# Kernel optimization log

Measured on AMD Instinct MI355X. Metric: run time of the kernel, lower is better.

## Reference

```python
import jax, jax.numpy as jnp
import numpy as np

B, N, D_MODEL, HIDDEN = 4, 1024, 1024, 1024
N_HEAD, D_KEY, D_VALUE = 16, 64, 64


def setup_inputs() -> dict:
    key = jax.random.key(0)
    ks = jax.random.split(key, 12)
    s = 0.02
    return {
        "queries": jax.random.normal(ks[0], (B, N, D_MODEL), jnp.float32),
        "keys": jax.random.normal(ks[1], (B, N, HIDDEN), jnp.float32),
        "values": jax.random.normal(ks[2], (B, N, HIDDEN), jnp.float32),
        "attn_bias": jax.random.normal(ks[3], (B, N_HEAD, N, N), jnp.float32),
        "Wq": jax.random.normal(ks[4], (D_MODEL, D_KEY * N_HEAD), jnp.float32) * s,
        "bq": jnp.zeros((D_KEY * N_HEAD,), jnp.float32),
        "Wk": jax.random.normal(ks[5], (HIDDEN, D_KEY * N_HEAD), jnp.float32) * s,
        "bk": jnp.zeros((D_KEY * N_HEAD,), jnp.float32),
        "Wv": jax.random.normal(ks[6], (HIDDEN, D_VALUE * N_HEAD), jnp.float32) * s,
        "bv": jnp.zeros((D_VALUE * N_HEAD,), jnp.float32),
        "Wo": jax.random.normal(ks[7], (max(D_MODEL, HIDDEN), D_MODEL), jnp.float32) * s,
        "bo": jnp.zeros((D_MODEL,), jnp.float32),
    }


def reference(queries, keys, values, attn_bias, Wq, bq, Wk, bk, Wv, bv, Wo, bo):
    b, n, _ = queries.shape
    # QKV projections, split heads -> [b, h, n, d]
    q = (queries @ Wq + bq).reshape(b, n, N_HEAD, D_KEY).transpose(0, 2, 1, 3)
    k = (keys @ Wk + bk).reshape(b, keys.shape[1], N_HEAD, D_KEY).transpose(0, 2, 1, 3)
    v = (values @ Wv + bv).reshape(b, values.shape[1], N_HEAD, D_VALUE).transpose(0, 2, 1, 3)
    # scaled dot-product attention with additive bias (dropout_rate=0 -> identity)
    scaled_q = q * (D_KEY ** -0.5)
    product = jnp.einsum("bhqd,bhkd->bhqk", scaled_q, k) + attn_bias
    weights = jax.nn.softmax(product, axis=-1)
    ctx = jnp.einsum("bhqk,bhkd->bhqd", weights, v)
    # combine heads -> [b, n, h*d]
    out = ctx.transpose(0, 2, 1, 3).reshape(b, n, N_HEAD * D_VALUE)
    return out @ Wo + bo
```

## Files before the change

### kernel.cpp

```cpp
#include <hip/hip_runtime.h>
#include <hip/hip_bf16.h>
#include <cstdint>
#include <type_traits>


typedef unsigned short u16;
typedef __attribute__((ext_vector_type(8))) short v8bf;
typedef __attribute__((ext_vector_type(4))) float v4f;

#define DEV static __device__ __forceinline__

DEV float b2f(u16 u) { union { uint32_t u; float f; } v; v.u = ((uint32_t)u) << 16; return v.f; }
DEV u16 f2b(float f) {
    union { float f; uint32_t u; } v; v.f = f;
    uint32_t r = v.u + 0x7FFFu + ((v.u >> 16) & 1u);
    return (u16)(r >> 16);
}

__global__ __launch_bounds__(256) void transpose_w(const float* __restrict__ in,
                                                   u16* __restrict__ out) {
    __shared__ float tile[32][33];
    const int tx = threadIdx.x, ty = threadIdx.y;
    const int n0 = blockIdx.x * 32, k0 = blockIdx.y * 32;
#pragma unroll
    for (int i = 0; i < 4; i++)
        tile[ty + i * 8][tx] = in[(size_t)(k0 + ty + i * 8) * 1024 + n0 + tx];
    __syncthreads();
#pragma unroll
    for (int i = 0; i < 4; i++)
        out[(size_t)(n0 + ty + i * 8) * 1024 + k0 + tx] = f2b(tile[tx][ty + i * 8]);
}

__global__ __launch_bounds__(256) void transpose_v(const u16* __restrict__ V,
                                                   u16* __restrict__ VT) {
    __shared__ u16 tile[32][33];
    const int tx = threadIdx.x, ty = threadIdx.y;
    const int n0 = blockIdx.x * 32, d0 = blockIdx.y * 32, bh = blockIdx.z;
    const int b = bh >> 4, h = bh & 15;
#pragma unroll
    for (int i = 0; i < 4; i++)
        tile[ty + i * 8][tx] = V[(size_t)(b * 1024 + n0 + ty + i * 8) * 1024 + h * 64 + d0 + tx];
    __syncthreads();
#pragma unroll
    for (int i = 0; i < 4; i++)
        VT[(size_t)(bh * 64 + d0 + ty + i * 8) * 1024 + n0 + tx] = tile[tx][ty + i * 8];
}

template <typename TA, typename TO>
__global__ __launch_bounds__(256) void gemm_nt(const TA* __restrict__ A,
                                               const u16* __restrict__ Bt,
                                               const float* __restrict__ bias,
                                               TO* __restrict__ C) {
    __shared__ __align__(16) u16 aS[128][72];
    __shared__ __align__(16) u16 bS[128][72];
    const int tid = threadIdx.x;
    const int wave = tid >> 6, lane = tid & 63;
    const int l16 = lane & 15, quad = lane >> 4;
    const int m0 = blockIdx.x * 128, n0 = blockIdx.y * 128;
    const int mb = (wave >> 1) * 64, nb = (wave & 1) * 64;

    v4f acc[4][4];
#pragma unroll
    for (int i = 0; i < 4; i++)
#pragma unroll
        for (int j = 0; j < 4; j++) acc[i][j] = (v4f){0.f, 0.f, 0.f, 0.f};

    for (int kk = 0; kk < 1024; kk += 64) {
        __syncthreads();
        if constexpr (std::is_same_v<TA, float>) {
#pragma unroll
            for (int i = 0; i < 8; i++) {
                const int idx = tid + 256 * i;
                const int row = idx >> 4, c4 = idx & 15;
                const float4 f = *reinterpret_cast<const float4*>(
                    &A[(size_t)(m0 + row) * 1024 + kk + c4 * 4]);
                union { u16 h[4]; uint2 v; } pk;
                pk.h[0] = f2b(f.x); pk.h[1] = f2b(f.y);
                pk.h[2] = f2b(f.z); pk.h[3] = f2b(f.w);
                *reinterpret_cast<uint2*>(&aS[row][c4 * 4]) = pk.v;
            }
        } else {
#pragma unroll
            for (int i = 0; i < 4; i++) {
                const int idx = tid + 256 * i;
                const int row = idx >> 3, off = idx & 7;
                *reinterpret_cast<int4*>(&aS[row][off * 8]) =
                    *reinterpret_cast<const int4*>(&A[(size_t)(m0 + row) * 1024 + kk + off * 8]);
            }
        }
#pragma unroll
        for (int i = 0; i < 4; i++) {
            const int idx = tid + 256 * i;
            const int row = idx >> 3, off = idx & 7;
            *reinterpret_cast<int4*>(&bS[row][off * 8]) =
                *reinterpret_cast<const int4*>(&Bt[(size_t)(n0 + row) * 1024 + kk + off * 8]);
        }
        __syncthreads();
#pragma unroll
        for (int kt = 0; kt < 2; kt++) {
            v8bf af[4], bfr[4];
#pragma unroll
            for (int i = 0; i < 4; i++) {
                af[i]  = *reinterpret_cast<const v8bf*>(&aS[mb + i * 16 + l16][kt * 32 + quad * 8]);
                bfr[i] = *reinterpret_cast<const v8bf*>(&bS[nb + i * 16 + l16][kt * 32 + quad * 8]);
            }
#pragma unroll
            for (int i = 0; i < 4; i++)
#pragma unroll
                for (int j = 0; j < 4; j++)
                    acc[i][j] = __builtin_amdgcn_mfma_f32_16x16x32_bf16(af[i], bfr[j], acc[i][j], 0, 0, 0);
        }
    }
    float bv[4];
#pragma unroll
    for (int j = 0; j < 4; j++) bv[j] = bias[n0 + nb + j * 16 + l16];
#pragma unroll
    for (int i = 0; i < 4; i++)
#pragma unroll
        for (int j = 0; j < 4; j++) {
            const int col = n0 + nb + j * 16 + l16;
#pragma unroll
            for (int r = 0; r < 4; r++) {
                const int row = m0 + mb + i * 16 + quad * 4 + r;
                const float val = acc[i][j][r] + bv[j];
                if constexpr (std::is_same_v<TO, u16>) C[(size_t)row * 1024 + col] = f2b(val);
                else                                   C[(size_t)row * 1024 + col] = val;
            }
        }
}

__global__ __launch_bounds__(256) void attn_kernel(const u16* __restrict__ Q,
                                                   const u16* __restrict__ K,
                                                   const u16* __restrict__ VT,
                                                   const float* __restrict__ bias,
                                                   u16* __restrict__ ctx) {
    __shared__ __align__(16) u16 kS[128][72];
    __shared__ __align__(16) u16 vS[64][136];
    __shared__ __align__(16) u16 pS[4][16][40];
    __shared__ float rsLDS[4][16];
    __shared__ float ctxLDS[4][16][64];

    const int tid = threadIdx.x;
    const int wave = tid >> 6, lane = tid & 63, l16 = lane & 15, quad = lane >> 4;
    const int q0 = blockIdx.x * 16;
    const int bh = blockIdx.y;
    const int b = bh >> 4, h = bh & 15;

    v8bf qf[2];
    {
        const size_t qrow = (size_t)(b * 1024 + q0 + l16) * 1024 + h * 64;
        qf[0] = *reinterpret_cast<const v8bf*>(&Q[qrow + quad * 8]);
        qf[1] = *reinterpret_cast<const v8bf*>(&Q[qrow + 32 + quad * 8]);
    }

    v4f ctxacc[4];
#pragma unroll
    for (int v = 0; v < 4; v++) ctxacc[v] = (v4f){0.f, 0.f, 0.f, 0.f};
    float rs[4] = {0.f, 0.f, 0.f, 0.f};

    const size_t kbase = (size_t)b * 1024 * 1024 + (size_t)h * 64;
    const size_t vtbase = (size_t)bh * 64 * 1024;
    const size_t bbase = ((size_t)bh * 1024 + q0) * 1024;

    for (int c = 0; c < 8; c++) {
        const int nc = c * 128;
        __syncthreads();
#pragma unroll
        for (int i = 0; i < 4; i++) {
            const int idx = tid + 256 * i;
            const int key = idx >> 3, off = idx & 7;
            *reinterpret_cast<int4*>(&kS[key][off * 8]) =
                *reinterpret_cast<const int4*>(&K[kbase + (size_t)(nc + key) * 1024 + off * 8]);
        }
#pragma unroll
        for (int i = 0; i < 4; i++) {
            const int idx = tid + 256 * i;
            const int d = idx >> 4, off = idx & 15;
            *reinterpret_cast<int4*>(&vS[d][off * 8]) =
                *reinterpret_cast<const int4*>(&VT[vtbase + (size_t)d * 1024 + nc + off * 8]);
        }
        __syncthreads();
#pragma unroll
        for (int t = 0; t < 2; t++) {
            v4f s = (v4f){0.f, 0.f, 0.f, 0.f};
#pragma unroll
            for (int kt = 0; kt < 2; kt++) {
                v8bf bfr = *reinterpret_cast<const v8bf*>(&kS[wave * 32 + t * 16 + l16][kt * 32 + quad * 8]);
                s = __builtin_amdgcn_mfma_f32_16x16x32_bf16(qf[kt], bfr, s, 0, 0, 0);
            }
            const int keyg = nc + wave * 32 + t * 16 + l16;
#pragma unroll
            for (int r = 0; r < 4; r++) {
                const float lg = s[r] * 0.125f + bias[bbase + (size_t)(quad * 4 + r) * 1024 + keyg];
                const float p = __expf(lg);
                rs[r] += p;
                pS[wave][quad * 4 + r][t * 16 + l16] = f2b(p);
            }
        }
        __syncthreads();
        {
            v8bf pf = *reinterpret_cast<const v8bf*>(&pS[wave][l16][quad * 8]);
#pragma unroll
            for (int v = 0; v < 4; v++) {
                v8bf vf = *reinterpret_cast<const v8bf*>(&vS[v * 16 + l16][wave * 32 + quad * 8]);
                ctxacc[v] = __builtin_amdgcn_mfma_f32_16x16x32_bf16(pf, vf, ctxacc[v], 0, 0, 0);
            }
        }
    }

#pragma unroll
    for (int r = 0; r < 4; r++) {
        float v = rs[r];
        v += __shfl_xor(v, 1, 16);
        v += __shfl_xor(v, 2, 16);
        v += __shfl_xor(v, 4, 16);
        v += __shfl_xor(v, 8, 16);
        rs[r] = v;
    }
    if (l16 == 0) {
#pragma unroll
        for (int r = 0; r < 4; r++) rsLDS[wave][quad * 4 + r] = rs[r];
    }
#pragma unroll
    for (int v = 0; v < 4; v++)
#pragma unroll
        for (int r = 0; r < 4; r++)
            ctxLDS[wave][quad * 4 + r][v * 16 + l16] = ctxacc[v][r];
    __syncthreads();
#pragma unroll
    for (int i = 0; i < 4; i++) {
        const int row = (tid >> 6) + 4 * i;
        const int d = tid & 63;
        const float sum = ctxLDS[0][row][d] + ctxLDS[1][row][d] + ctxLDS[2][row][d] + ctxLDS[3][row][d];
        const float den = rsLDS[0][row] + rsLDS[1][row] + rsLDS[2][row] + rsLDS[3][row];
        ctx[(size_t)(b * 1024 + q0 + row) * 1024 + h * 64 + d] = f2b(sum / den);
    }
}

extern "C" void kernel_launch(void* const* d_in, const int* in_sizes, int n_in,
                              void* d_out, int out_size, void* d_ws, size_t ws_size,
                              hipStream_t stream) {
    const float* queries = (const float*)d_in[0];
    const float* keys    = (const float*)d_in[1];
    const float* values  = (const float*)d_in[2];
    const float* abias   = (const float*)d_in[3];
    const float* Wq = (const float*)d_in[4];
    const float* bq = (const float*)d_in[5];
    const float* Wk = (const float*)d_in[6];
    const float* bk = (const float*)d_in[7];
    const float* Wv = (const float*)d_in[8];
    const float* bv = (const float*)d_in[9];
    const float* Wo = (const float*)d_in[10];
    const float* bo = (const float*)d_in[11];
    float* out = (float*)d_out;

    char* ws = (char*)d_ws;
    u16* Qb   = (u16*)(ws);
    u16* Kb   = (u16*)(ws + (size_t)(8u << 20));
    u16* Vb   = (u16*)(ws + (size_t)(16u << 20));
    u16* VTb  = (u16*)(ws + (size_t)(24u << 20));
    u16* ctxb = (u16*)(ws + (size_t)(32u << 20));
    u16* WqT  = (u16*)(ws + (size_t)(40u << 20));
    u16* WkT  = (u16*)(ws + (size_t)(42u << 20));
    u16* WvT  = (u16*)(ws + (size_t)(44u << 20));
    u16* WoT  = (u16*)(ws + (size_t)(46u << 20));

    dim3 tb(32, 8);
    transpose_w<<<dim3(32, 32), tb, 0, stream>>>(Wq, WqT);
    transpose_w<<<dim3(32, 32), tb, 0, stream>>>(Wk, WkT);
    transpose_w<<<dim3(32, 32), tb, 0, stream>>>(Wv, WvT);
    transpose_w<<<dim3(32, 32), tb, 0, stream>>>(Wo, WoT);

    gemm_nt<float, u16><<<dim3(32, 8), 256, 0, stream>>>(queries, WqT, bq, Qb);
    gemm_nt<float, u16><<<dim3(32, 8), 256, 0, stream>>>(keys,    WkT, bk, Kb);
    gemm_nt<float, u16><<<dim3(32, 8), 256, 0, stream>>>(values,  WvT, bv, Vb);

    transpose_v<<<dim3(32, 2, 64), tb, 0, stream>>>(Vb, VTb);

    attn_kernel<<<dim3(64, 64), 256, 0, stream>>>(Qb, Kb, VTb, abias, ctxb);

    gemm_nt<u16, float><<<dim3(32, 8), 256, 0, stream>>>(ctxb, WoT, bo, out);
}
```

Before: 586.6 us.

## Give each attention wave its own query rows and batch weight transposes and QKV GEMMs

The attention kernel now gives each block 64 query rows, with each wave owning 16 rows and sweeping all 128 keys of a chunk. This reuses every K/V tile loaded into LDS across four times more queries and drops the cross-wave LDS reduction of context and row sums. The four weight transposes become one launch and the three QKV GEMMs become one launch, cutting launch count and letting the blocks fill the device together. In exchange the attention grid shrinks four-fold to 1024 blocks, and per-wave register and LDS use grows.

```diff
diff --git a/kernel.cpp b/kernel.cpp
--- a/kernel.cpp
+++ b/kernel.cpp
@@ -17,9 +17,18 @@
     return (u16)(r >> 16);
 }
 
-__global__ __launch_bounds__(256) void transpose_w(const float* __restrict__ in,
-                                                   u16* __restrict__ out) {
+__global__ __launch_bounds__(256) void transpose_w4(const float* __restrict__ w0,
+                                                    const float* __restrict__ w1,
+                                                    const float* __restrict__ w2,
+                                                    const float* __restrict__ w3,
+                                                    u16* __restrict__ o0,
+                                                    u16* __restrict__ o1,
+                                                    u16* __restrict__ o2,
+                                                    u16* __restrict__ o3) {
     __shared__ float tile[32][33];
+    const int z = blockIdx.z;
+    const float* in = (z == 0) ? w0 : (z == 1) ? w1 : (z == 2) ? w2 : w3;
+    u16* out = (z == 0) ? o0 : (z == 1) ? o1 : (z == 2) ? o2 : o3;
     const int tx = threadIdx.x, ty = threadIdx.y;
     const int n0 = blockIdx.x * 32, k0 = blockIdx.y * 32;
 #pragma unroll
@@ -47,16 +56,14 @@
 }
 
 template <typename TA, typename TO>
-__global__ __launch_bounds__(256) void gemm_nt(const TA* __restrict__ A,
-                                               const u16* __restrict__ Bt,
-                                               const float* __restrict__ bias,
-                                               TO* __restrict__ C) {
+DEV void gemm_body(const TA* __restrict__ A, const u16* __restrict__ Bt,
+                   const float* __restrict__ bias, TO* __restrict__ C,
+                   int m0, int n0) {
     __shared__ __align__(16) u16 aS[128][72];
     __shared__ __align__(16) u16 bS[128][72];
     const int tid = threadIdx.x;
     const int wave = tid >> 6, lane = tid & 63;
     const int l16 = lane & 15, quad = lane >> 4;
-    const int m0 = blockIdx.x * 128, n0 = blockIdx.y * 128;
     const int mb = (wave >> 1) * 64, nb = (wave & 1) * 64;
 
     v4f acc[4][4];
@@ -129,38 +136,64 @@
         }
 }
 
+__global__ __launch_bounds__(256) void gemm_qkv(const float* __restrict__ q,
+                                                const float* __restrict__ k,
+                                                const float* __restrict__ v,
+                                                const u16* __restrict__ WqT,
+                                                const u16* __restrict__ WkT,
+                                                const u16* __restrict__ WvT,
+                                                const float* __restrict__ bq,
+                                                const float* __restrict__ bk,
+                                                const float* __restrict__ bv,
+                                                u16* __restrict__ Qb,
+                                                u16* __restrict__ Kb,
+                                                u16* __restrict__ Vb) {
+    const int z = blockIdx.z;
+    const float* A = (z == 0) ? q : (z == 1) ? k : v;
+    const u16* Bt  = (z == 0) ? WqT : (z == 1) ? WkT : WvT;
+    const float* bi = (z == 0) ? bq : (z == 1) ? bk : bv;
+    u16* C = (z == 0) ? Qb : (z == 1) ? Kb : Vb;
+    gemm_body<float, u16>(A, Bt, bi, C, blockIdx.x * 128, blockIdx.y * 128);
+}
+
+__global__ __launch_bounds__(256) void gemm_out(const u16* __restrict__ A,
+                                                const u16* __restrict__ Bt,
+                                                const float* __restrict__ bias,
+                                                float* __restrict__ C) {
+    gemm_body<u16, float>(A, Bt, bias, C, blockIdx.x * 128, blockIdx.y * 128);
+}
+
 __global__ __launch_bounds__(256) void attn_kernel(const u16* __restrict__ Q,
                                                    const u16* __restrict__ K,
                                                    const u16* __restrict__ VT,
                                                    const float* __restrict__ bias,
                                                    u16* __restrict__ ctx) {
     __shared__ __align__(16) u16 kS[128][72];
-    __shared__ __align__(16) u16 vS[64][136];
-    __shared__ __align__(16) u16 pS[4][16][40];
-    __shared__ float rsLDS[4][16];
-    __shared__ float ctxLDS[4][16][64];
+    __shared__ __align__(16) u16 vS[64][132];
+    __shared__ __align__(16) u16 pS[4][16][132];
 
     const int tid = threadIdx.x;
     const int wave = tid >> 6, lane = tid & 63, l16 = lane & 15, quad = lane >> 4;
-    const int q0 = blockIdx.x * 16;
+    const int q0 = blockIdx.x * 64;
     const int bh = blockIdx.y;
     const int b = bh >> 4, h = bh & 15;
+    const int qw = q0 + wave * 16;
 
     v8bf qf[2];
     {
-        const size_t qrow = (size_t)(b * 1024 + q0 + l16) * 1024 + h * 64;
+        const size_t qrow = (size_t)(b * 1024 + qw + l16) * 1024 + h * 64;
         qf[0] = *reinterpret_cast<const v8bf*>(&Q[qrow + quad * 8]);
         qf[1] = *reinterpret_cast<const v8bf*>(&Q[qrow + 32 + quad * 8]);
     }
 
-    v4f ctxacc[4];
-#pragma unroll
-    for (int v = 0; v < 4; v++) ctxacc[v] = (v4f){0.f, 0.f, 0.f, 0.f};
+    v4f ctxa[4];
+#pragma unroll
+    for (int dt = 0; dt < 4; dt++) ctxa[dt] = (v4f){0.f, 0.f, 0.f, 0.f};
     float rs[4] = {0.f, 0.f, 0.f, 0.f};
 
     const size_t kbase = (size_t)b * 1024 * 1024 + (size_t)h * 64;
     const size_t vtbase = (size_t)bh * 64 * 1024;
-    const size_t bbase = ((size_t)bh * 1024 + q0) * 1024;
+    const size_t bbase = ((size_t)bh * 1024 + qw) * 1024;
 
     for (int c = 0; c < 8; c++) {
         const int nc = c * 128;
@@ -181,14 +214,14 @@
         }
         __syncthreads();
 #pragma unroll
-        for (int t = 0; t < 2; t++) {
+        for (int t = 0; t < 8; t++) {
             v4f s = (v4f){0.f, 0.f, 0.f, 0.f};
 #pragma unroll
             for (int kt = 0; kt < 2; kt++) {
-                v8bf bfr = *reinterpret_cast<const v8bf*>(&kS[wave * 32 + t * 16 + l16][kt * 32 + quad * 8]);
+                v8bf bfr = *reinterpret_cast<const v8bf*>(&kS[t * 16 + l16][kt * 32 + quad * 8]);
                 s = __builtin_amdgcn_mfma_f32_16x16x32_bf16(qf[kt], bfr, s, 0, 0, 0);
             }
-            const int keyg = nc + wave * 32 + t * 16 + l16;
+            const int keyg = nc + t * 16 + l16;
 #pragma unroll
             for (int r = 0; r < 4; r++) {
                 const float lg = s[r] * 0.125f + bias[bbase + (size_t)(quad * 4 + r) * 1024 + keyg];
@@ -198,12 +231,13 @@
             }
         }
         __syncthreads();
-        {
-            v8bf pf = *reinterpret_cast<const v8bf*>(&pS[wave][l16][quad * 8]);
-#pragma unroll
-            for (int v = 0; v < 4; v++) {
-                v8bf vf = *reinterpret_cast<const v8bf*>(&vS[v * 16 + l16][wave * 32 + quad * 8]);
-                ctxacc[v] = __builtin_amdgcn_mfma_f32_16x16x32_bf16(pf, vf, ctxacc[v], 0, 0, 0);
+#pragma unroll
+        for (int kt = 0; kt < 4; kt++) {
+            v8bf pf = *reinterpret_cast<const v8bf*>(&pS[wave][l16][kt * 32 + quad * 8]);
+#pragma unroll
+            for (int dt = 0; dt < 4; dt++) {
+                v8bf vf = *reinterpret_cast<const v8bf*>(&vS[dt * 16 + l16][kt * 32 + quad * 8]);
+                ctxa[dt] = __builtin_amdgcn_mfma_f32_16x16x32_bf16(pf, vf, ctxa[dt], 0, 0, 0);
             }
         }
     }
@@ -215,26 +249,16 @@
         v += __shfl_xor(v, 2, 16);
         v += __shfl_xor(v, 4, 16);
         v += __shfl_xor(v, 8, 16);
-        rs[r] = v;
+        rs[r] = 1.0f / v;
     }
-    if (l16 == 0) {
-#pragma unroll
-        for (int r = 0; r < 4; r++) rsLDS[wave][quad * 4 + r] = rs[r];
-    }
-#pragma unroll
-    for (int v = 0; v < 4; v++)
-#pragma unroll
-        for (int r = 0; r < 4; r++)
-            ctxLDS[wave][quad * 4 + r][v * 16 + l16] = ctxacc[v][r];
-    __syncthreads();
-#pragma unroll
-    for (int i = 0; i < 4; i++) {
-        const int row = (tid >> 6) + 4 * i;
-        const int d = tid & 63;
-        const float sum = ctxLDS[0][row][d] + ctxLDS[1][row][d] + ctxLDS[2][row][d] + ctxLDS[3][row][d];
-        const float den = rsLDS[0][row] + rsLDS[1][row] + rsLDS[2][row] + rsLDS[3][row];
-        ctx[(size_t)(b * 1024 + q0 + row) * 1024 + h * 64 + d] = f2b(sum / den);
-    }
+#pragma unroll
+    for (int dt = 0; dt < 4; dt++)
+#pragma unroll
+        for (int r = 0; r < 4; r++) {
+            const int row = qw + quad * 4 + r;
+            const int d = dt * 16 + l16;
+            ctx[(size_t)(b * 1024 + row) * 1024 + h * 64 + d] = f2b(ctxa[dt][r] * rs[r]);
+        }
 }
 
 extern "C" void kernel_launch(void* const* d_in, const int* in_sizes, int n_in,
@@ -265,19 +289,16 @@
     u16* WvT  = (u16*)(ws + (size_t)(44u << 20));
     u16* WoT  = (u16*)(ws + (size_t)(46u << 20));
 
-    dim3 tb(32, 8);
-    transpose_w<<<dim3(32, 32), tb, 0, stream>>>(Wq, WqT);
-    transpose_w<<<dim3(32, 32), tb, 0, stream>>>(Wk, WkT);
-    transpose_w<<<dim3(32, 32), tb, 0, stream>>>(Wv, WvT);
-    transpose_w<<<dim3(32, 32), tb, 0, stream>>>(Wo, WoT);
-
-    gemm_nt<float, u16><<<dim3(32, 8), 256, 0, stream>>>(queries, WqT, bq, Qb);
-    gemm_nt<float, u16><<<dim3(32, 8), 256, 0, stream>>>(keys,    WkT, bk, Kb);
-    gemm_nt<float, u16><<<dim3(32, 8), 256, 0, stream>>>(values,  WvT, bv, Vb);
-
-    transpose_v<<<dim3(32, 2, 64), tb, 0, stream>>>(Vb, VTb);
-
-    attn_kernel<<<dim3(64, 64), 256, 0, stream>>>(Qb, Kb, VTb, abias, ctxb);
-
-    gemm_nt<u16, float><<<dim3(32, 8), 256, 0, stream>>>(ctxb, WoT, bo, out);
-}
+    transpose_w4<<<dim3(32, 32, 4), dim3(32, 8), 0, stream>>>(Wq, Wk, Wv, Wo,
+                                                              WqT, WkT, WvT, WoT);
+
+    gemm_qkv<<<dim3(32, 8, 3), 256, 0, stream>>>(queries, keys, values,
+                                                 WqT, WkT, WvT, bq, bk, bv,
+                                                 Qb, Kb, Vb);
+
+    transpose_v<<<dim3(32, 2, 64), dim3(32, 8), 0, stream>>>(Vb, VTb);
+
+    attn_kernel<<<dim3(16, 64), 256, 0, stream>>>(Qb, Kb, VTb, abias, ctxb);
+
+    gemm_out<<<dim3(32, 8), 256, 0, stream>>>(ctxb, WoT, bo, out);
+}
```

Result: slower. 694.7 us (+18.4%).
